# Kernel tuning notes

Measured on AMD Instinct MI355X. Metric: run time of the kernel, lower is better.

The kernel has to match this reference:

```python
import jax, jax.numpy as jnp
import numpy as np

EPS = 1e-7  # dummy-column epsilon from stanza utils.add_dummy(eps=True)


def setup_inputs() -> dict:
    key = jax.random.key(0)
    ks = jax.random.split(key, 9)
    n_mentions, emb = 10000, 1024
    batch, n_ants, pw_emb = 1024, 64, 64
    hidden = 1024
    in_features = 3 * emb + pw_emb  # 3136
    return {
        "all_mentions": jax.random.normal(ks[0], (n_mentions, emb), jnp.float32),
        "mentions_batch": jax.random.normal(ks[1], (batch, emb), jnp.float32),
        "pw_batch": jax.random.normal(ks[2], (batch, n_ants, pw_emb), jnp.float32),
        "top_indices_batch": jax.random.randint(ks[3], (batch, n_ants), 0, n_mentions),
        "top_rough_scores_batch": jax.random.normal(ks[4], (batch, n_ants), jnp.float32),
        "W1": jax.random.normal(ks[5], (hidden, in_features), jnp.float32) * 0.02,
        "b1": jax.random.normal(ks[6], (hidden,), jnp.float32) * 0.02,
        "Wout": jax.random.normal(ks[7], (1, hidden), jnp.float32) * 0.02,
        "bout": jax.random.normal(ks[8], (1,), jnp.float32) * 0.02,
    }


def reference(all_mentions, mentions_batch, pw_batch, top_indices_batch,
              top_rough_scores_batch, W1, b1, Wout, bout):
    n_ants = pw_batch.shape[1]
    # pair matrix: [batch, n_ants, 3*emb + pw_emb]
    a = jnp.broadcast_to(mentions_batch[:, None, :],
                         (mentions_batch.shape[0], n_ants, mentions_batch.shape[1]))
    b = all_mentions[top_indices_batch]          # gather: [batch, n_ants, emb]
    pair = jnp.concatenate((a, b, a * b, pw_batch), axis=2)
    # FFNN: Linear -> LeakyReLU (dropout is identity at eval) -> Linear(->1)
    h = jax.nn.leaky_relu(jnp.einsum('bnf,hf->bnh', pair, W1) + b1, negative_slope=0.01)
    ffnn = (jnp.einsum('bnh,oh->bno', h, Wout) + bout)[..., 0]  # [batch, n_ants]
    scores = top_rough_scores_batch + ffnn
    # add dummy column with eps at position 0 -> [batch, n_ants + 1]
    dummy = jnp.full((scores.shape[0], 1), EPS, scores.dtype)
    return jnp.concatenate((dummy, scores), axis=1)
```

## Files before the change

### kernel.cpp

```cpp
#include <hip/hip_runtime.h>
#include <hip/hip_bf16.h>
#include <cstdint>
#include <cstdio>

typedef unsigned short u16;
typedef unsigned int   u32;
typedef __attribute__((ext_vector_type(8))) short bf16x8;
typedef __attribute__((ext_vector_type(4))) float f32x4;
typedef __attribute__((ext_vector_type(4))) u16   u16x4;
typedef __attribute__((ext_vector_type(8))) u16   u16x8;

#define GLOBAL_AS __attribute__((address_space(1)))
#define LDS_AS    __attribute__((address_space(3)))

static __device__ __forceinline__ u16 f2bf(float f) {
  u32 u = __builtin_bit_cast(u32, f);
  u = (u + 0x7fffu + ((u >> 16) & 1u)) >> 16;
  return (u16)u;
}
static __device__ __forceinline__ float bf2f(u16 v) {
  return __builtin_bit_cast(float, (u32)v << 16);
}
static __device__ __forceinline__ void gload_lds16(const void* g, void* l) {
  __builtin_amdgcn_global_load_lds((GLOBAL_AS u32*)g, (LDS_AS u32*)l, 16, 0, 0);
}

__global__ void k_cvt(const float* __restrict__ src, int ld, int c0,
                      int rows_src, int cols4, int total4,
                      u16* __restrict__ dst, int ldd, int dcol) {
  int gid = blockIdx.x * 256 + threadIdx.x;
  if (gid >= total4) return;
  int r = gid / cols4;
  int c = (gid - r * cols4) * 4;
  u16x4 o = {0, 0, 0, 0};
  if (r < rows_src) {
    const float4 v = *(const float4*)&src[(size_t)r * ld + c0 + c];
    o[0] = f2bf(v.x); o[1] = f2bf(v.y); o[2] = f2bf(v.z); o[3] = f2bf(v.w);
  }
  *(u16x4*)&dst[(size_t)r * ldd + dcol + c] = o;
}

__global__ void k_init(const float* __restrict__ rough,
                       const float* __restrict__ bout,
                       float* __restrict__ out) {
  int i = blockIdx.x * 256 + threadIdx.x;
  if (i >= 1024 * 65) return;
  int bi = i / 65, c = i - bi * 65;
  out[i] = (c == 0) ? 1e-7f : rough[bi * 64 + c - 1] + bout[0];
}

__global__ __launch_bounds__(256)
void gemm128(const u16* __restrict__ A, int lda,
             const u16* __restrict__ B, int ldb, int Ksteps,
             u16* __restrict__ C, int ldc, const float* __restrict__ bias) {
  __shared__ u16 As[128 * 64];
  __shared__ u16 Bs[128 * 64];
  const int t = threadIdx.x;
  const int w = t >> 6, l = t & 63;
  const int wr = w >> 1, wc = w & 1;
  const int brow = blockIdx.x * 128;
  const int bcol = blockIdx.y * 128;
  const int srow = t >> 3;
  const int scol = (t & 7) * 8;
  const int gsw  = (((t & 7) ^ ((t >> 3) & 7))) * 8;

  f32x4 acc[4][4] = {};
  for (int ks = 0; ks < Ksteps; ++ks) {
    const int kb = ks * 64;
#pragma unroll
    for (int q = 0; q < 4; ++q) {
      int r = q * 32 + srow;
      gload_lds16(A + (size_t)(brow + r) * lda + kb + gsw, &As[r * 64 + scol]);
      gload_lds16(B + (size_t)(bcol + r) * ldb + kb + gsw, &Bs[r * 64 + scol]);
    }
    __syncthreads();
#pragma unroll
    for (int kk = 0; kk < 2; ++kk) {
      bf16x8 af[4], bfr[4];
      const int pg = ((kk * 4 + (l >> 4)) ^ (l & 7)) * 8;
#pragma unroll
      for (int m = 0; m < 4; ++m)
        af[m] = *(const bf16x8*)&As[(wr * 64 + m * 16 + (l & 15)) * 64 + pg];
#pragma unroll
      for (int n = 0; n < 4; ++n)
        bfr[n] = *(const bf16x8*)&Bs[(wc * 64 + n * 16 + (l & 15)) * 64 + pg];
#pragma unroll
      for (int m = 0; m < 4; ++m)
#pragma unroll
        for (int n = 0; n < 4; ++n)
          acc[m][n] = __builtin_amdgcn_mfma_f32_16x16x32_bf16(af[m], bfr[n], acc[m][n], 0, 0, 0);
    }
    __syncthreads();
  }
#pragma unroll
  for (int m = 0; m < 4; ++m)
#pragma unroll
    for (int n = 0; n < 4; ++n)
#pragma unroll
      for (int reg = 0; reg < 4; ++reg) {
        int row = brow + wr * 64 + m * 16 + (l >> 4) * 4 + reg;
        int col = bcol + wc * 64 + n * 16 + (l & 15);
        float v = acc[m][n][reg] + (bias ? bias[col] : 0.f);
        C[(size_t)row * ldc + col] = f2bf(v);
      }
}

template<bool FUSED>
__global__ __launch_bounds__(512, 1)
void gemm256(const u16* __restrict__ A, int lda,
             const u16* __restrict__ B, int ldb, int NT,
             u16* __restrict__ C, int ldc,
             const u16* __restrict__ a16, const u16* __restrict__ allm16,
             const float* __restrict__ pw,
             const u16* __restrict__ Aproj, const u16* __restrict__ Bproj,
             const float* __restrict__ Wout,
             const int* __restrict__ topidx, float* __restrict__ out) {
  extern __shared__ u16 lds[];
  u16* As = lds;
  u16* Bs = lds + 2 * 2 * 128 * 64;
  u16* a16lds = Bs + 2 * 256 * 64;

  const int t = threadIdx.x;
  const int l = t & 63;
  const int w = t >> 6;
  const int wrow = w >> 2, wcol = w & 3;
  const int brow = blockIdx.x * 256;
  const int bcol = blockIdx.y * 256;

  const int sr  = t >> 3;
  const int sc  = (t & 7) * 8;
  const int gsw = ((t & 7) ^ (sr & 7)) * 8;

  int mi_[2][2], grow_[2][2];
  if constexpr (FUSED) {
#pragma unroll
    for (int h = 0; h < 2; ++h)
#pragma unroll
      for (int s = 0; s < 2; ++s) {
        int lr = sr + 64 * s;
        int g  = ((lr >> 5) << 6) + h * 32 + (lr & 31);
        grow_[h][s] = brow + g;
        mi_[h][s]   = topidx[brow + g];
      }
  }

  auto stageA = [&](int kt, int h) {
    if (kt >= NT) return;
#pragma unroll
    for (int s = 0; s < 2; ++s) {
      int lr = sr + 64 * s;
      int g  = ((lr >> 5) << 6) + h * 32 + (lr & 31);
      gload_lds16(A + (size_t)(brow + g) * lda + kt * 64 + gsw,
                  &As[(((kt & 1) * 2 + h) * 128 + lr) * 64 + sc]);
    }
  };
  auto stageRawA = [&](int kt, int h) {
    if (kt >= NT) return;
#pragma unroll
    for (int s = 0; s < 2; ++s) {
      int lr = sr + 64 * s;
      gload_lds16(allm16 + (size_t)mi_[h][s] * 1024 + kt * 64 + gsw,
                  &As[(((kt & 1) * 2 + h) * 128 + lr) * 64 + sc]);
    }
  };
  auto stageB = [&](int kt, int h) {
    if (kt >= NT) return;
#pragma unroll
    for (int s = 0; s < 2; ++s) {
      int lr = h * 128 + sr + 64 * s;
      gload_lds16(B + (size_t)(bcol + lr) * ldb + kt * 64 + gsw,
                  &Bs[((kt & 1) * 256 + lr) * 64 + sc]);
    }
  };
  auto rmwA = [&](int kt1, int h) {
    if (kt1 >= NT) return;
    const int cb = kt1 & 1;
    if (kt1 == NT - 1) {
#pragma unroll
      for (int s = 0; s < 2; ++s) {
        int lr = sr + 64 * s;
        const float* p = &pw[(size_t)grow_[h][s] * 64 + gsw];
        float4 p0 = *(const float4*)p;
        float4 p1 = *(const float4*)(p + 4);
        u16x8 o;
        o[0] = f2bf(p0.x); o[1] = f2bf(p0.y); o[2] = f2bf(p0.z); o[3] = f2bf(p0.w);
        o[4] = f2bf(p1.x); o[5] = f2bf(p1.y); o[6] = f2bf(p1.z); o[7] = f2bf(p1.w);
        *(u16x8*)&As[((cb * 2 + h) * 128 + lr) * 64 + sc] = o;
      }
    } else {
#pragma unroll
      for (int s = 0; s < 2; ++s) {
        int lr = sr + 64 * s;
        u16x8 b = *(const u16x8*)&As[((cb * 2 + h) * 128 + lr) * 64 + sc];
        u16x8 a = *(const u16x8*)&a16lds[(lr >> 5) * 1024 + kt1 * 64 + gsw];
        u16x8 o;
#pragma unroll
        for (int j = 0; j < 8; ++j) o[j] = f2bf(bf2f(a[j]) * bf2f(b[j]));
        *(u16x8*)&As[((cb * 2 + h) * 128 + lr) * 64 + sc] = o;
      }
    }
  };

  f32x4 acc[8][4] = {};

  if constexpr (FUSED) {
    gload_lds16(&a16[(size_t)((brow >> 6) + (t >> 7)) * 1024 + (t & 127) * 8],
                &a16lds[(size_t)t * 8]);
    stageB(0, 0); stageB(0, 1); stageRawA(0, 0); stageRawA(0, 1);
    stageB(1, 0); stageB(1, 1);
    asm volatile("s_waitcnt vmcnt(6)" ::: "memory");
    rmwA(0, 0);
    asm volatile("s_waitcnt lgkmcnt(0)" ::: "memory");
  } else {
    stageB(0, 0); stageB(0, 1); stageA(0, 0); stageA(0, 1);
    stageB(1, 0); stageB(1, 1);
    asm volatile("s_waitcnt vmcnt(6)" ::: "memory");
  }
  __builtin_amdgcn_s_barrier();

  for (int kt = 0; kt < NT; ++kt) {
    const int cbuf = kt & 1;
    bf16x8 bfr[4][2];
#pragma unroll
    for (int q = 0; q < 4; ++q) {
      if (q == 0) {
#pragma unroll
        for (int n = 0; n < 4; ++n) {
          int row = wcol * 64 + n * 16 + (l & 15);
#pragma unroll
          for (int kk = 0; kk < 2; ++kk) {
            int gran = (kk * 4 + (l >> 4)) ^ (l & 7);
            bfr[n][kk] = *(const bf16x8*)&Bs[(cbuf * 256 + row) * 64 + gran * 8];
          }
        }
      }
      bf16x8 af[2][2];
#pragma unroll
      for (int m2 = 0; m2 < 2; ++m2) {
        int m = 2 * q + m2;
        int g = wrow * 128 + m * 16 + (l & 15);
        int lra = ((g >> 6) << 5) + (g & 31);
#pragma unroll
        for (int kk = 0; kk < 2; ++kk) {
          int gran = (kk * 4 + (l >> 4)) ^ (l & 7);
          af[m2][kk] = *(const bf16x8*)&As[((cbuf * 2 + (q & 1)) * 128 + lra) * 64 + gran * 8];
        }
      }

      if constexpr (FUSED) {
        if      (q == 0) stageRawA(kt + 1, 0);
        else if (q == 1) stageRawA(kt + 1, 1);
        else if (q == 2) stageB(kt + 2, 0);
        else             stageB(kt + 2, 1);
      } else {
        if      (q == 0) stageA(kt + 1, 0);
        else if (q == 1) stageA(kt + 1, 1);
        else if (q == 2) stageB(kt + 2, 0);
        else             stageB(kt + 2, 1);
      }

      if (q == 0) asm volatile("s_waitcnt lgkmcnt(8)" ::: "memory");
      __builtin_amdgcn_s_barrier();
      asm volatile("s_waitcnt lgkmcnt(0)" ::: "memory");
      __builtin_amdgcn_sched_barrier(0);
      __builtin_amdgcn_s_setprio(1);
#pragma unroll
      for (int m2 = 0; m2 < 2; ++m2)
#pragma unroll
        for (int n = 0; n < 4; ++n)
#pragma unroll
          for (int kk = 0; kk < 2; ++kk)
            acc[2 * q + m2][n] = __builtin_amdgcn_mfma_f32_16x16x32_bf16(
                af[m2][kk], bfr[n][kk], acc[2 * q + m2][n], 0, 0, 0);
      __builtin_amdgcn_s_setprio(0);

      if (q == 0) {
        if (kt + 1 < NT) asm volatile("s_waitcnt vmcnt(6)" ::: "memory");
        else             asm volatile("s_waitcnt vmcnt(0)" ::: "memory");
        if constexpr (FUSED) {
          rmwA(kt, 1);
          asm volatile("s_waitcnt lgkmcnt(0)" ::: "memory");
        }
      } else if (q == 3 && kt + 1 < NT) {
        if (kt + 2 < NT) asm volatile("s_waitcnt vmcnt(6)" ::: "memory");
        else             asm volatile("s_waitcnt vmcnt(2)" ::: "memory");
        if constexpr (FUSED) {
          rmwA(kt + 1, 0);
          asm volatile("s_waitcnt lgkmcnt(0)" ::: "memory");
        }
      }
      __builtin_amdgcn_s_barrier();
    }
  }

  if constexpr (FUSED) {
    __syncthreads();
    u16* Pb = lds;
#pragma unroll
    for (int pass = 0; pass < 16; ++pass) {
      int rr = pass * 16 + (t >> 5);
      int mi = topidx[brow + rr];
      int cc = (t & 31) * 8;
      int scc = cc ^ (((rr >> 1) & 7) << 3);
      gload_lds16(&Bproj[(size_t)mi * 1024 + bcol + scc], &Pb[rr * 256 + cc]);
    }
    asm volatile("s_waitcnt vmcnt(0)" ::: "memory");
    __syncthreads();

    float wo[4], av[2][4];
    const int bi0 = (brow >> 6) + wrow * 2;
#pragma unroll
    for (int n = 0; n < 4; ++n) {
      int col = bcol + wcol * 64 + n * 16 + (l & 15);
      wo[n] = Wout[col];
#pragma unroll
      for (int j = 0; j < 2; ++j)
        av[j][n] = bf2f(Aproj[(size_t)(bi0 + j) * 1024 + col]);
    }
#pragma unroll
    for (int m = 0; m < 8; ++m) {
#pragma unroll
      for (int reg = 0; reg < 4; ++reg) {
        int lrow = wrow * 128 + m * 16 + (l >> 4) * 4 + reg;
        int gr = brow + lrow;
        int key = ((lrow >> 1) & 7) << 3;
        float s = 0.f;
#pragma unroll
        for (int n = 0; n < 4; ++n) {
          int lcol = wcol * 64 + n * 16 + (l & 15);
          float v = acc[m][n][reg] + av[m >> 2][n] + bf2f(Pb[lrow * 256 + (lcol ^ key)]);
          v = v > 0.f ? v : 0.01f * v;
          s += v * wo[n];
        }
        s += __shfl_xor(s, 1);
        s += __shfl_xor(s, 2);
        s += __shfl_xor(s, 4);
        s += __shfl_xor(s, 8);
        if ((l & 15) == 0)
          atomicAdd(&out[(gr >> 6) * 65 + 1 + (gr & 63)], s);
      }
    }
  } else {
#pragma unroll
    for (int m = 0; m < 8; ++m)
#pragma unroll
      for (int n = 0; n < 4; ++n)
#pragma unroll
        for (int reg = 0; reg < 4; ++reg) {
          int row = brow + wrow * 128 + m * 16 + (l >> 4) * 4 + reg;
          int col = bcol + wcol * 64 + n * 16 + (l & 15);
          C[(size_t)row * ldc + col] = f2bf(acc[m][n][reg]);
        }
  }
}

extern "C" void kernel_launch(void* const* d_in, const int* in_sizes, int n_in,
                              void* d_out, int out_size, void* d_ws, size_t ws_size,
                              hipStream_t stream) {
  const float* allm  = (const float*)d_in[0];
  const float* ments = (const float*)d_in[1];
  const float* pw    = (const float*)d_in[2];
  const int*   tidx  = (const int*)d_in[3];
  const float* rough = (const float*)d_in[4];
  const float* W1    = (const float*)d_in[5];
  const float* b1    = (const float*)d_in[6];
  const float* Wout  = (const float*)d_in[7];
  const float* bout  = (const float*)d_in[8];
  float* out = (float*)d_out;

  u16* A16    = (u16*)d_ws;
  u16* allm16 = A16 + 1024 * 1024;
  u16* W1a    = allm16 + 10240 * 1024;
  u16* W1b    = W1a + 1024 * 1024;
  u16* W1cp   = W1b + 1024 * 1024;
  u16* Aproj  = W1cp + 1024 * 1088;
  u16* Bproj  = Aproj + 1024 * 1024;

  size_t need = (size_t)2 * ((size_t)1024*1024 + 10240*1024 + 1024*1024 + 1024*1024
              + 1024*1088 + 1024*1024 + 10240*1024);
  if (ws_size < need) {
    fprintf(stderr, "kernel_launch: ws_size %zu < needed %zu\n", ws_size, need);
    return;
  }

  hipFuncSetAttribute((const void*)&gemm256<false>,
                      hipFuncAttributeMaxDynamicSharedMemorySize, 131072);
  hipFuncSetAttribute((const void*)&gemm256<true>,
                      hipFuncAttributeMaxDynamicSharedMemorySize, 139264);

  {
    int t4;
    t4 = 1024 * 256;
    k_cvt<<<(t4 + 255) / 256, 256, 0, stream>>>(W1, 3136, 0,    1024, 256, t4, W1a, 1024, 0);
    k_cvt<<<(t4 + 255) / 256, 256, 0, stream>>>(W1, 3136, 1024, 1024, 256, t4, W1b, 1024, 0);
    k_cvt<<<(t4 + 255) / 256, 256, 0, stream>>>(W1, 3136, 2048, 1024, 256, t4, W1cp, 1088, 0);
    t4 = 1024 * 16;
    k_cvt<<<(t4 + 255) / 256, 256, 0, stream>>>(W1, 3136, 3072, 1024, 16, t4, W1cp, 1088, 1024);
    t4 = 1024 * 256;
    k_cvt<<<(t4 + 255) / 256, 256, 0, stream>>>(ments, 1024, 0, 1024, 256, t4, A16, 1024, 0);
    t4 = 10240 * 256;
    k_cvt<<<(t4 + 255) / 256, 256, 0, stream>>>(allm, 1024, 0, 10000, 256, t4, allm16, 1024, 0);
  }

  gemm128<<<dim3(8, 8), 256, 0, stream>>>(A16, 1024, W1a, 1024, 16, Aproj, 1024, b1);
  gemm256<false><<<dim3(40, 4), 512, 131072, stream>>>(allm16, 1024, W1b, 1024, 16,
                                                       Bproj, 1024,
                                                       nullptr, nullptr, nullptr,
                                                       nullptr, nullptr, nullptr,
                                                       nullptr, nullptr);

  k_init<<<260, 256, 0, stream>>>(rough, bout, out);

  gemm256<true><<<dim3(256, 4), 512, 139264, stream>>>(nullptr, 0, W1cp, 1088, 17,
                                                       nullptr, 0,
                                                       A16, allm16, pw,
                                                       Aproj, Bproj, Wout,
                                                       tidx, out);
}
```

Measured before the change: 320.7 us.

## Sort pair rows by gathered mention index to improve gather locality

Adds a counting sort (histogram, scan, scatter) that orders all pair rows by their antecedent mention index, so blocks of the fused GEMM gather nearby or identical all_mentions rows and Bproj rows. Because rows are now permuted, the per-batch a16 tile in LDS is replaced by per-thread register loads of the mention row. Aproj is now fetched per output row, and outputs are scattered through the permutation. pw is pre-converted to bf16 and loaded via direct-to-LDS loads instead of a float read-modify-write. This adds three small kernels and an extra conversion pass, plus less regular access to a16 and Aproj.

```diff
diff --git a/kernel.cpp b/kernel.cpp
--- a/kernel.cpp
+++ b/kernel.cpp
@@ -47,6 +47,39 @@
   if (i >= 1024 * 65) return;
   int bi = i / 65, c = i - bi * 65;
   out[i] = (c == 0) ? 1e-7f : rough[bi * 64 + c - 1] + bout[0];
+}
+
+__global__ void k_hist(const int* __restrict__ tidx, int* __restrict__ cnt) {
+  int i = blockIdx.x * 256 + threadIdx.x;
+  atomicAdd(&cnt[tidx[i]], 1);
+}
+
+__global__ void k_scan(int* __restrict__ cnt) {
+  __shared__ int part[512];
+  int t = threadIdx.x;
+  int local[20], s = 0;
+#pragma unroll
+  for (int i = 0; i < 20; ++i) { local[i] = cnt[t * 20 + i]; s += local[i]; }
+  part[t] = s;
+  __syncthreads();
+  for (int off = 1; off < 512; off <<= 1) {
+    int v = (t >= off) ? part[t - off] : 0;
+    __syncthreads();
+    part[t] += v;
+    __syncthreads();
+  }
+  int ex = part[t] - s;
+#pragma unroll
+  for (int i = 0; i < 20; ++i) { int c = local[i]; cnt[t * 20 + i] = ex; ex += c; }
+}
+
+__global__ void k_scatter(const int* __restrict__ tidx, int* __restrict__ cnt,
+                          int* __restrict__ perm, int* __restrict__ miS) {
+  int i = blockIdx.x * 256 + threadIdx.x;
+  int mi = tidx[i];
+  int pos = atomicAdd(&cnt[mi], 1);
+  perm[pos] = i;
+  miS[pos] = mi;
 }
 
 __global__ __launch_bounds__(256)
@@ -111,14 +144,14 @@
              const u16* __restrict__ B, int ldb, int NT,
              u16* __restrict__ C, int ldc,
              const u16* __restrict__ a16, const u16* __restrict__ allm16,
-             const float* __restrict__ pw,
+             const u16* __restrict__ pwb,
              const u16* __restrict__ Aproj, const u16* __restrict__ Bproj,
              const float* __restrict__ Wout,
-             const int* __restrict__ topidx, float* __restrict__ out) {
+             const int* __restrict__ perm, const int* __restrict__ miS,
+             float* __restrict__ out) {
   extern __shared__ u16 lds[];
   u16* As = lds;
   u16* Bs = lds + 2 * 2 * 128 * 64;
-  u16* a16lds = Bs + 2 * 256 * 64;
 
   const int t = threadIdx.x;
   const int l = t & 63;
@@ -131,7 +164,7 @@
   const int sc  = (t & 7) * 8;
   const int gsw = ((t & 7) ^ (sr & 7)) * 8;
 
-  int mi_[2][2], grow_[2][2];
+  int mi_[2][2], pair_[2][2];
   if constexpr (FUSED) {
 #pragma unroll
     for (int h = 0; h < 2; ++h)
@@ -139,8 +172,8 @@
       for (int s = 0; s < 2; ++s) {
         int lr = sr + 64 * s;
         int g  = ((lr >> 5) << 6) + h * 32 + (lr & 31);
-        grow_[h][s] = brow + g;
-        mi_[h][s]   = topidx[brow + g];
+        pair_[h][s] = perm[brow + g];
+        mi_[h][s]   = miS[brow + g];
       }
   }
 
@@ -159,8 +192,10 @@
 #pragma unroll
     for (int s = 0; s < 2; ++s) {
       int lr = sr + 64 * s;
-      gload_lds16(allm16 + (size_t)mi_[h][s] * 1024 + kt * 64 + gsw,
-                  &As[(((kt & 1) * 2 + h) * 128 + lr) * 64 + sc]);
+      const u16* src = (kt == NT - 1)
+          ? (pwb + (size_t)pair_[h][s] * 64 + gsw)
+          : (allm16 + (size_t)mi_[h][s] * 1024 + kt * 64 + gsw);
+      gload_lds16(src, &As[(((kt & 1) * 2 + h) * 128 + lr) * 64 + sc]);
     }
   };
   auto stageB = [&](int kt, int h) {
@@ -172,44 +207,35 @@
                   &Bs[((kt & 1) * 256 + lr) * 64 + sc]);
     }
   };
-  auto rmwA = [&](int kt1, int h) {
-    if (kt1 >= NT) return;
+  auto issueM = [&](int kt1, int h, u16x8* am) {
+    if (kt1 >= NT - 1) return;
+#pragma unroll
+    for (int s = 0; s < 2; ++s)
+      am[s] = *(const u16x8*)&a16[(size_t)(pair_[h][s] >> 6) * 1024 + kt1 * 64 + gsw];
+  };
+  auto rmwFin = [&](int kt1, int h, const u16x8* am) {
+    if (kt1 >= NT - 1) return;
     const int cb = kt1 & 1;
-    if (kt1 == NT - 1) {
-#pragma unroll
-      for (int s = 0; s < 2; ++s) {
-        int lr = sr + 64 * s;
-        const float* p = &pw[(size_t)grow_[h][s] * 64 + gsw];
-        float4 p0 = *(const float4*)p;
-        float4 p1 = *(const float4*)(p + 4);
-        u16x8 o;
-        o[0] = f2bf(p0.x); o[1] = f2bf(p0.y); o[2] = f2bf(p0.z); o[3] = f2bf(p0.w);
-        o[4] = f2bf(p1.x); o[5] = f2bf(p1.y); o[6] = f2bf(p1.z); o[7] = f2bf(p1.w);
-        *(u16x8*)&As[((cb * 2 + h) * 128 + lr) * 64 + sc] = o;
-      }
-    } else {
-#pragma unroll
-      for (int s = 0; s < 2; ++s) {
-        int lr = sr + 64 * s;
-        u16x8 b = *(const u16x8*)&As[((cb * 2 + h) * 128 + lr) * 64 + sc];
-        u16x8 a = *(const u16x8*)&a16lds[(lr >> 5) * 1024 + kt1 * 64 + gsw];
-        u16x8 o;
-#pragma unroll
-        for (int j = 0; j < 8; ++j) o[j] = f2bf(bf2f(a[j]) * bf2f(b[j]));
-        *(u16x8*)&As[((cb * 2 + h) * 128 + lr) * 64 + sc] = o;
-      }
+#pragma unroll
+    for (int s = 0; s < 2; ++s) {
+      int lr = sr + 64 * s;
+      u16x8 b = *(const u16x8*)&As[((cb * 2 + h) * 128 + lr) * 64 + sc];
+      u16x8 o;
+#pragma unroll
+      for (int j = 0; j < 8; ++j) o[j] = f2bf(bf2f(am[s][j]) * bf2f(b[j]));
+      *(u16x8*)&As[((cb * 2 + h) * 128 + lr) * 64 + sc] = o;
     }
   };
 
   f32x4 acc[8][4] = {};
 
   if constexpr (FUSED) {
-    gload_lds16(&a16[(size_t)((brow >> 6) + (t >> 7)) * 1024 + (t & 127) * 8],
-                &a16lds[(size_t)t * 8]);
+    u16x8 am0[2];
+    issueM(0, 0, am0);
     stageB(0, 0); stageB(0, 1); stageRawA(0, 0); stageRawA(0, 1);
     stageB(1, 0); stageB(1, 1);
     asm volatile("s_waitcnt vmcnt(6)" ::: "memory");
-    rmwA(0, 0);
+    rmwFin(0, 0, am0);
     asm volatile("s_waitcnt lgkmcnt(0)" ::: "memory");
   } else {
     stageB(0, 0); stageB(0, 1); stageA(0, 0); stageA(0, 1);
@@ -221,6 +247,7 @@
   for (int kt = 0; kt < NT; ++kt) {
     const int cbuf = kt & 1;
     bf16x8 bfr[4][2];
+    u16x8 am1[2], am0n[2];
 #pragma unroll
     for (int q = 0; q < 4; ++q) {
       if (q == 0) {
@@ -248,10 +275,10 @@
       }
 
       if constexpr (FUSED) {
-        if      (q == 0) stageRawA(kt + 1, 0);
-        else if (q == 1) stageRawA(kt + 1, 1);
-        else if (q == 2) stageB(kt + 2, 0);
-        else             stageB(kt + 2, 1);
+        if      (q == 0) { issueM(kt, 1, am1); stageRawA(kt + 1, 0); }
+        else if (q == 1) { stageRawA(kt + 1, 1); }
+        else if (q == 2) { stageB(kt + 2, 0); }
+        else             { issueM(kt + 1, 0, am0n); stageB(kt + 2, 1); }
       } else {
         if      (q == 0) stageA(kt + 1, 0);
         else if (q == 1) stageA(kt + 1, 1);
@@ -278,14 +305,14 @@
         if (kt + 1 < NT) asm volatile("s_waitcnt vmcnt(6)" ::: "memory");
         else             asm volatile("s_waitcnt vmcnt(0)" ::: "memory");
         if constexpr (FUSED) {
-          rmwA(kt, 1);
+          rmwFin(kt, 1, am1);
           asm volatile("s_waitcnt lgkmcnt(0)" ::: "memory");
         }
       } else if (q == 3 && kt + 1 < NT) {
         if (kt + 2 < NT) asm volatile("s_waitcnt vmcnt(6)" ::: "memory");
         else             asm volatile("s_waitcnt vmcnt(2)" ::: "memory");
         if constexpr (FUSED) {
-          rmwA(kt + 1, 0);
+          rmwFin(kt + 1, 0, am0n);
           asm volatile("s_waitcnt lgkmcnt(0)" ::: "memory");
         }
       }
@@ -299,7 +326,7 @@
 #pragma unroll
     for (int pass = 0; pass < 16; ++pass) {
       int rr = pass * 16 + (t >> 5);
-      int mi = topidx[brow + rr];
+      int mi = miS[brow + rr];
       int cc = (t & 31) * 8;
       int scc = cc ^ (((rr >> 1) & 7) << 3);
       gload_lds16(&Bproj[(size_t)mi * 1024 + bcol + scc], &Pb[rr * 256 + cc]);
@@ -307,28 +334,24 @@
     asm volatile("s_waitcnt vmcnt(0)" ::: "memory");
     __syncthreads();
 
-    float wo[4], av[2][4];
-    const int bi0 = (brow >> 6) + wrow * 2;
-#pragma unroll
-    for (int n = 0; n < 4; ++n) {
-      int col = bcol + wcol * 64 + n * 16 + (l & 15);
-      wo[n] = Wout[col];
-#pragma unroll
-      for (int j = 0; j < 2; ++j)
-        av[j][n] = bf2f(Aproj[(size_t)(bi0 + j) * 1024 + col]);
-    }
+    float wo[4];
+#pragma unroll
+    for (int n = 0; n < 4; ++n)
+      wo[n] = Wout[bcol + wcol * 64 + n * 16 + (l & 15)];
 #pragma unroll
     for (int m = 0; m < 8; ++m) {
 #pragma unroll
       for (int reg = 0; reg < 4; ++reg) {
         int lrow = wrow * 128 + m * 16 + (l >> 4) * 4 + reg;
-        int gr = brow + lrow;
+        int pr = perm[brow + lrow];
+        int bi = pr >> 6;
         int key = ((lrow >> 1) & 7) << 3;
         float s = 0.f;
 #pragma unroll
         for (int n = 0; n < 4; ++n) {
           int lcol = wcol * 64 + n * 16 + (l & 15);
-          float v = acc[m][n][reg] + av[m >> 2][n] + bf2f(Pb[lrow * 256 + (lcol ^ key)]);
+          float v = acc[m][n][reg] + bf2f(Aproj[(size_t)bi * 1024 + bcol + lcol])
+                  + bf2f(Pb[lrow * 256 + (lcol ^ key)]);
           v = v > 0.f ? v : 0.01f * v;
           s += v * wo[n];
         }
@@ -337,7 +360,7 @@
         s += __shfl_xor(s, 4);
         s += __shfl_xor(s, 8);
         if ((l & 15) == 0)
-          atomicAdd(&out[(gr >> 6) * 65 + 1 + (gr & 63)], s);
+          atomicAdd(&out[bi * 65 + 1 + (pr & 63)], s);
       }
     }
   } else {
@@ -375,9 +398,14 @@
   u16* W1cp   = W1b + 1024 * 1024;
   u16* Aproj  = W1cp + 1024 * 1088;
   u16* Bproj  = Aproj + 1024 * 1024;
+  u16* pwb    = Bproj + 10240 * 1024;
+  int* cnt    = (int*)(pwb + (size_t)65536 * 64);
+  int* perm   = cnt + 10240;
+  int* miS    = perm + 65536;
 
   size_t need = (size_t)2 * ((size_t)1024*1024 + 10240*1024 + 1024*1024 + 1024*1024
-              + 1024*1088 + 1024*1024 + 10240*1024);
+              + 1024*1088 + 1024*1024 + 10240*1024 + (size_t)65536*64)
+              + (size_t)4 * (10240 + 65536 + 65536);
   if (ws_size < need) {
     fprintf(stderr, "kernel_launch: ws_size %zu < needed %zu\n", ws_size, need);
     return;
@@ -386,7 +414,12 @@
   hipFuncSetAttribute((const void*)&gemm256<false>,
                       hipFuncAttributeMaxDynamicSharedMemorySize, 131072);
   hipFuncSetAttribute((const void*)&gemm256<true>,
-                      hipFuncAttributeMaxDynamicSharedMemorySize, 139264);
+                      hipFuncAttributeMaxDynamicSharedMemorySize, 131072);
+
+  hipMemsetAsync(cnt, 0, 10240 * sizeof(int), stream);
+  k_hist<<<256, 256, 0, stream>>>(tidx, cnt);
+  k_scan<<<1, 512, 0, stream>>>(cnt);
+  k_scatter<<<256, 256, 0, stream>>>(tidx, cnt, perm, miS);
 
   {
     int t4;
@@ -400,6 +433,8 @@
     k_cvt<<<(t4 + 255) / 256, 256, 0, stream>>>(ments, 1024, 0, 1024, 256, t4, A16, 1024, 0);
     t4 = 10240 * 256;
     k_cvt<<<(t4 + 255) / 256, 256, 0, stream>>>(allm, 1024, 0, 10000, 256, t4, allm16, 1024, 0);
+    t4 = 65536 * 16;
+    k_cvt<<<(t4 + 255) / 256, 256, 0, stream>>>(pw, 64, 0, 65536, 16, t4, pwb, 64, 0);
   }
 
   gemm128<<<dim3(8, 8), 256, 0, stream>>>(A16, 1024, W1a, 1024, 16, Aproj, 1024, b1);
@@ -407,13 +442,13 @@
                                                        Bproj, 1024,
                                                        nullptr, nullptr, nullptr,
                                                        nullptr, nullptr, nullptr,
-                                                       nullptr, nullptr);
+                                                       nullptr, nullptr, nullptr);
 
   k_init<<<260, 256, 0, stream>>>(rough, bout, out);
 
-  gemm256<true><<<dim3(256, 4), 512, 139264, stream>>>(nullptr, 0, W1cp, 1088, 17,
+  gemm256<true><<<dim3(256, 4), 512, 131072, stream>>>(nullptr, 0, W1cp, 1088, 17,
                                                        nullptr, 0,
-                                                       A16, allm16, pw,
+                                                       A16, allm16, pwb,
                                                        Aproj, Bproj, Wout,
-                                                       tidx, out);
-}
+                                                       perm, miS, out);
+}
```

New measurement: 390.8 us. +21.9%, slower.
